# Performance work log

Measured on AMD Instinct MI355X. Metric: run time of the kernel, lower is better.

The kernel has to match this reference:

```python
import jax, jax.numpy as jnp
import numpy as np

V, EH, EO, H, O = 32000, 512, 256, 512, 256
S, B = 128, 32
THRESH = 1e-6


def _uniform(key, shape, fan_in):
    bound = 1.0 / np.sqrt(fan_in)
    return jax.random.uniform(key, shape, jnp.float32, -bound, bound)


def setup_inputs() -> dict:
    key = jax.random.key(0)
    ks = jax.random.split(key, 12)
    return {
        "input": jax.random.randint(ks[0], (S, B), 0, V, dtype=jnp.int32),
        # embedding_layer: Linear(V,EH), Linear(EH,EO); stored (in,out)
        "W1": _uniform(ks[1], (V, EH), V),
        "b1": _uniform(ks[2], (EH,), V),
        "W2": _uniform(ks[3], (EH, EO), EH),
        "b2": _uniform(ks[4], (EO,), EH),
        # GRU weights (PyTorch layout: gates stacked r,z,n)
        "W_ih": _uniform(ks[5], (3 * H, EO), H),
        "W_hh": _uniform(ks[6], (3 * H, H), H),
        "b_ih": _uniform(ks[7], (3 * H,), H),
        "b_hh": _uniform(ks[8], (3 * H,), H),
        # head: Linear(H,O)
        "W3": _uniform(ks[9], (H, O), H),
        "b3": _uniform(ks[10], (O,), H),
    }


def reference(input, W1, b1, W2, b2, W_ih, W_hh, b_ih, b_hh, W3, b3):
    thr = lambda x: jnp.where(x > THRESH, x, 0.0)  # nn.Threshold(1e-6, 0)
    # one_hot(input, V) @ W1 == row gather of W1 (same math, no O(V) GEMM)
    emb = thr(thr(W1[input] + b1) @ W2 + b2)  # (S, B, EO)

    # GRU: precompute input projections for all timesteps
    x_proj = emb @ W_ih.T + b_ih  # (S, B, 3H)
    h0 = jnp.zeros((B, H), jnp.float32)

    def step(h, xp):
        gh = h @ W_hh.T + b_hh
        xr, xz, xn = jnp.split(xp, 3, axis=-1)
        hr, hz, hn = jnp.split(gh, 3, axis=-1)
        r = jax.nn.sigmoid(xr + hr)
        z = jax.nn.sigmoid(xz + hz)
        n = jnp.tanh(xn + r * hn)
        h_new = (1.0 - z) * n + z * h
        return h_new, None

    hT, _ = jax.lax.scan(step, h0, x_proj)  # final hidden (B, H)
    # linear head on h_n (dropout in eval mode = identity); torch h_n is (1,B,H)
    out = hT[None, :, :] @ W3 + b3  # (1, B, O)
    return out
```

## Files before the change

kernel.cpp:

```cpp
#include <hip/hip_runtime.h>
#include <cstddef>

#define THRESH 1e-6f
#define SPIN_LIMIT (1 << 20)

__device__ __forceinline__ float thrf(float x) { return x > THRESH ? x : 0.0f; }
__device__ __forceinline__ float sigm(float x) { return 1.0f / (1.0f + expf(-x)); }
__device__ __forceinline__ void fma4(float4& c, float a, float4 b) {
    c.x += a * b.x; c.y += a * b.y; c.z += a * b.z; c.w += a * b.w;
}
__device__ __forceinline__ void macc4(float4& a, float4 w, float4 h) {
    a.x += w.x * h.x; a.y += w.y * h.y; a.z += w.z * h.z; a.w += w.w * h.w;
}
__device__ __forceinline__ float hsum4(float4 a) { return a.x + a.y + a.z + a.w; }

__global__ __launch_bounds__(256) void k_embed_gemm(const int* __restrict__ tok,
                                                    const float* __restrict__ W1,
                                                    const float* __restrict__ b1,
                                                    const float* __restrict__ W2,
                                                    const float* __restrict__ b2,
                                                    float* __restrict__ emb) {
    constexpr int BM = 64, BN = 64, BK = 32, K = 512, N = 256;
    __shared__ float As[BK][BM + 1];
    __shared__ float Bs[BK][BN];

    const int tid = threadIdx.x;
    const int bm = blockIdx.x * BM;
    const int bn = blockIdx.y * BN;
    const int tn = (tid & 15) * 4;
    const int tm = (tid >> 4) * 4;

    float acc[4][4] = {};

    for (int k0 = 0; k0 < K; k0 += BK) {
        for (int i = tid; i < BM * BK / 4; i += 256) {
            int c4 = (i & (BK / 4 - 1)) * 4;
            int r  = i / (BK / 4);
            int tv = tok[bm + r];
            float4 v  = *(const float4*)(W1 + (size_t)tv * K + k0 + c4);
            float4 bb = *(const float4*)(b1 + k0 + c4);
            As[c4 + 0][r] = thrf(v.x + bb.x);
            As[c4 + 1][r] = thrf(v.y + bb.y);
            As[c4 + 2][r] = thrf(v.z + bb.z);
            As[c4 + 3][r] = thrf(v.w + bb.w);
        }
        for (int i = tid; i < BK * BN / 4; i += 256) {
            int n4 = (i & 15) * 4;
            int kk = i >> 4;
            *(float4*)&Bs[kk][n4] = *(const float4*)(W2 + (size_t)(k0 + kk) * N + bn + n4);
        }
        __syncthreads();

        for (int k = 0; k < BK; ++k) {
            float a0 = As[k][tm + 0], a1 = As[k][tm + 1];
            float a2 = As[k][tm + 2], a3 = As[k][tm + 3];
            float b0 = Bs[k][tn + 0], b1v = Bs[k][tn + 1];
            float b2v = Bs[k][tn + 2], b3v = Bs[k][tn + 3];
            acc[0][0] += a0 * b0;  acc[0][1] += a0 * b1v;
            acc[0][2] += a0 * b2v; acc[0][3] += a0 * b3v;
            acc[1][0] += a1 * b0;  acc[1][1] += a1 * b1v;
            acc[1][2] += a1 * b2v; acc[1][3] += a1 * b3v;
            acc[2][0] += a2 * b0;  acc[2][1] += a2 * b1v;
            acc[2][2] += a2 * b2v; acc[2][3] += a2 * b3v;
            acc[3][0] += a3 * b0;  acc[3][1] += a3 * b1v;
            acc[3][2] += a3 * b2v; acc[3][3] += a3 * b3v;
        }
        __syncthreads();
    }

    const float4 bv = *(const float4*)(b2 + bn + tn);
    for (int i = 0; i < 4; ++i) {
        int m = bm + tm + i;
        float4 o;
        o.x = thrf(acc[i][0] + bv.x);
        o.y = thrf(acc[i][1] + bv.y);
        o.z = thrf(acc[i][2] + bv.z);
        o.w = thrf(acc[i][3] + bv.w);
        *(float4*)(emb + (size_t)m * N + bn + tn) = o;
    }
}

__global__ __launch_bounds__(256) void k_xproj(const float* __restrict__ emb,
                                               const float* __restrict__ W_ih,
                                               const float* __restrict__ b_ih,
                                               float* __restrict__ xp) {
    constexpr int BM = 128, BJ = 64, BK = 32, K = 256, J = 1536;
    __shared__ __align__(16) float As[BK][BM + 4];
    __shared__ __align__(16) float Bs[BK][BJ + 4];
    const int tid = threadIdx.x;
    const int bm = blockIdx.x * BM;
    const int bj = blockIdx.y * BJ;
    const int tj = (tid & 15) * 4;
    const int tm = (tid >> 4) * 8;

    float4 acc[8];
#pragma unroll
    for (int i = 0; i < 8; ++i) acc[i] = make_float4(0.f, 0.f, 0.f, 0.f);

    for (int k0 = 0; k0 < K; k0 += BK) {
#pragma unroll
        for (int p = 0; p < 4; ++p) {
            int i = tid + p * 256;
            int c4 = (i & 7) * 4, r = i >> 3;
            float4 v = *(const float4*)(emb + (size_t)(bm + r) * K + k0 + c4);
            As[c4 + 0][r] = v.x; As[c4 + 1][r] = v.y;
            As[c4 + 2][r] = v.z; As[c4 + 3][r] = v.w;
        }
#pragma unroll
        for (int p = 0; p < 2; ++p) {
            int i = tid + p * 256;
            int c4 = (i & 7) * 4, r = i >> 3;
            float4 v = *(const float4*)(W_ih + (size_t)(bj + r) * K + k0 + c4);
            Bs[c4 + 0][r] = v.x; Bs[c4 + 1][r] = v.y;
            Bs[c4 + 2][r] = v.z; Bs[c4 + 3][r] = v.w;
        }
        __syncthreads();

#pragma unroll 8
        for (int k = 0; k < BK; ++k) {
            float4 b4 = *(const float4*)&Bs[k][tj];
            float4 a0 = *(const float4*)&As[k][tm];
            float4 a1 = *(const float4*)&As[k][tm + 4];
            fma4(acc[0], a0.x, b4); fma4(acc[1], a0.y, b4);
            fma4(acc[2], a0.z, b4); fma4(acc[3], a0.w, b4);
            fma4(acc[4], a1.x, b4); fma4(acc[5], a1.y, b4);
            fma4(acc[6], a1.z, b4); fma4(acc[7], a1.w, b4);
        }
        __syncthreads();
    }

    const float4 bb = *(const float4*)(b_ih + bj + tj);
#pragma unroll
    for (int i = 0; i < 8; ++i) {
        float4 o = make_float4(acc[i].x + bb.x, acc[i].y + bb.y,
                               acc[i].z + bb.z, acc[i].w + bb.w);
        *(float4*)(xp + (size_t)(bm + tm + i) * J + bj + tj) = o;
    }
}

__global__ __launch_bounds__(256) void k_scan(const float* __restrict__ xp,
                                              const float* __restrict__ W_hh,
                                              const float* __restrict__ b_hh,
                                              unsigned long long* __restrict__ hx,
                                              float* __restrict__ h_out) {
    constexpr int HS = 520;
    __shared__ __align__(16) float hl[4][HS];
    __shared__ float red[4][16][12];

    const int tid = threadIdx.x;
    const int g   = blockIdx.x & 7;
    const int m   = blockIdx.x >> 3;
    const int jl  = tid & 15;
    const int kc  = tid >> 4;
    const int jglob = m * 16 + jl;

    float4 wr[8], wz[8], wn[8];
#pragma unroll
    for (int i = 0; i < 8; ++i) {
        const int k = kc * 4 + i * 64;
        wr[i] = *(const float4*)(W_hh + (size_t)jglob * 512 + k);
        wz[i] = *(const float4*)(W_hh + (size_t)(512 + jglob) * 512 + k);
        wn[i] = *(const float4*)(W_hh + (size_t)(1024 + jglob) * 512 + k);
    }

    const int jf  = tid & 15;
    const int bf  = (tid >> 4) & 3;
    const int jfg = m * 16 + jf;
    const int bg  = g * 4 + bf;
    float bhr = 0.f, bhz = 0.f, bhn = 0.f, hprev = 0.f;
    if (tid < 64) {
        bhr = b_hh[jfg];
        bhz = b_hh[512 + jfg];
        bhn = b_hh[1024 + jfg];
    }

    for (int i = tid; i < 4 * HS; i += 256) ((float*)hl)[i] = 0.f;
    __syncthreads();

    for (int t = 0; t < 128; ++t) {
        float xr = 0.f, xz = 0.f, xn = 0.f;
        if (tid < 64) {
            const float* xrow = xp + (size_t)(t * 32 + bg) * 1536;
            xr = xrow[jfg];
            xz = xrow[512 + jfg];
            xn = xrow[1024 + jfg];
        }

        if (t > 0) {
            const unsigned tag = (unsigned)t;
            unsigned long long* base = hx + (size_t)(t & 1) * 16384 + (size_t)(g * 4) * 512;
            unsigned long long v[8];
#pragma unroll
            for (int p = 0; p < 8; ++p)
                v[p] = __hip_atomic_load(base + tid + 256 * p,
                                         __ATOMIC_RELAXED, __HIP_MEMORY_SCOPE_AGENT);
            int spins = 0;
            for (;;) {
                bool all = true;
#pragma unroll
                for (int p = 0; p < 8; ++p) {
                    if ((unsigned)(v[p] >> 32) != tag) {
                        all = false;
                        v[p] = __hip_atomic_load(base + tid + 256 * p,
                                                 __ATOMIC_RELAXED, __HIP_MEMORY_SCOPE_AGENT);
                    }
                }
                if (all || ++spins > SPIN_LIMIT) break;
                __builtin_amdgcn_s_sleep(1);
            }
#pragma unroll
            for (int p = 0; p < 8; ++p) {
                const int flat = tid + 256 * p;
                union { unsigned u; float f; } cv;
                cv.u = (unsigned)v[p];
                hl[flat >> 9][flat & 511] = cv.f;
            }
            __syncthreads();
        }

        float p[3][4];
#pragma unroll
        for (int b = 0; b < 4; ++b) {
            float4 ar = make_float4(0.f, 0.f, 0.f, 0.f), az = ar, an = ar;
#pragma unroll
            for (int i = 0; i < 8; ++i) {
                float4 h4 = *(const float4*)&hl[b][kc * 4 + i * 64];
                macc4(ar, wr[i], h4);
                macc4(az, wz[i], h4);
                macc4(an, wn[i], h4);
            }
            p[0][b] = hsum4(ar); p[1][b] = hsum4(az); p[2][b] = hsum4(an);
        }

#pragma unroll
        for (int gg = 0; gg < 3; ++gg)
#pragma unroll
            for (int b = 0; b < 4; ++b) {
                float v = p[gg][b];
                v += __shfl_xor(v, 16);
                v += __shfl_xor(v, 32);
                p[gg][b] = v;
            }
        if ((tid & 48) == 0) {
            const int w = tid >> 6;
#pragma unroll
            for (int gg = 0; gg < 3; ++gg)
#pragma unroll
                for (int b = 0; b < 4; ++b)
                    red[w][jl][gg * 4 + b] = p[gg][b];
        }
        __syncthreads();

        if (tid < 64) {
            float sr = bhr, sz = bhz, sn = bhn;
#pragma unroll
            for (int w = 0; w < 4; ++w) {
                sr += red[w][jf][0 + bf];
                sz += red[w][jf][4 + bf];
                sn += red[w][jf][8 + bf];
            }
            float r  = sigm(xr + sr);
            float z  = sigm(xz + sz);
            float n  = tanhf(xn + r * sn);
            float hn = (1.0f - z) * n + z * hprev;
            hprev = hn;
            if (t < 127) {
                union { float f; unsigned u; } cv;
                cv.f = hn;
                const unsigned long long pk =
                    ((unsigned long long)(unsigned)(t + 1) << 32) | cv.u;
                __hip_atomic_store(hx + (size_t)((t + 1) & 1) * 16384 + (size_t)bg * 512 + jfg,
                                   pk, __ATOMIC_RELAXED, __HIP_MEMORY_SCOPE_AGENT);
            } else {
                h_out[(size_t)bg * 512 + jfg] = hn;
            }
        }
    }
}

__global__ __launch_bounds__(256) void k_head(const float* __restrict__ h,
                                              const float* __restrict__ W3,
                                              const float* __restrict__ b3,
                                              float* __restrict__ out) {
    const int b = blockIdx.x;
    const int o = threadIdx.x;
    const float* hrow = h + (size_t)b * 512;
    float acc = b3[o];
#pragma unroll 8
    for (int k = 0; k < 512; ++k)
        acc += hrow[k] * W3[(size_t)k * 256 + o];
    out[(size_t)b * 256 + o] = acc;
}

extern "C" void kernel_launch(void* const* d_in, const int* in_sizes, int n_in,
                              void* d_out, int out_size, void* d_ws, size_t ws_size,
                              hipStream_t stream) {
    const int*   tok  = (const int*)d_in[0];
    const float* W1   = (const float*)d_in[1];
    const float* b1   = (const float*)d_in[2];
    const float* W2   = (const float*)d_in[3];
    const float* b2   = (const float*)d_in[4];
    const float* W_ih = (const float*)d_in[5];
    const float* W_hh = (const float*)d_in[6];
    const float* b_ih = (const float*)d_in[7];
    const float* b_hh = (const float*)d_in[8];
    const float* W3   = (const float*)d_in[9];
    const float* b3   = (const float*)d_in[10];
    float* out = (float*)d_out;
    (void)ws_size;

    float* ws   = (float*)d_ws;
    float* emb  = ws;
    float* xp   = ws + 1048576;
    unsigned long long* hx = (unsigned long long*)(ws + 7340032);
    float* hfin = ws + 7340032 + 65536;

    {
        dim3 grd(4096 / 64, 256 / 64);
        k_embed_gemm<<<grd, 256, 0, stream>>>(tok, W1, b1, W2, b2, emb);
    }
    {
        dim3 grd(4096 / 128, 1536 / 64);
        k_xproj<<<grd, 256, 0, stream>>>(emb, W_ih, b_ih, xp);
    }
    k_scan<<<256, 256, 0, stream>>>(xp, W_hh, b_hh, hx, hfin);

    k_head<<<32, 256, 0, stream>>>(hfin, W3, b3, out);
}
```

Measured before the change: 708.7 us.

## Restructure GRU scan: 512-thread blocks, in-wave reduction, double-buffered hidden state

The persistent GRU scan moves from 256 blocks of 256 threads to 128 blocks of 512. Each wave now owns 4 hidden units, and the K dimension is split across 16 lanes, so the gate dot products are reduced with wave shuffles. This removes the shared-memory reduction array and one block barrier per timestep. The hidden state is staged in double-buffered, padded LDS with float4 stores, so only one barrier per step remains. The trade-off is fewer blocks, which means fewer producers and consumers per sync, but more threads per block and more shuffle steps.

Result: slower. 940.3 us (+32.7%).

```diff
diff --git a/kernel.cpp b/kernel.cpp
--- a/kernel.cpp
+++ b/kernel.cpp
@@ -138,93 +138,93 @@
     }
 }
 
-__global__ __launch_bounds__(256) void k_scan(const float* __restrict__ xp,
+__global__ __launch_bounds__(512) void k_scan(const float* __restrict__ xp,
                                               const float* __restrict__ W_hh,
                                               const float* __restrict__ b_hh,
                                               unsigned long long* __restrict__ hx,
                                               float* __restrict__ h_out) {
-    constexpr int HS = 520;
-    __shared__ __align__(16) float hl[4][HS];
-    __shared__ float red[4][16][12];
-
-    const int tid = threadIdx.x;
-    const int g   = blockIdx.x & 7;
-    const int m   = blockIdx.x >> 3;
-    const int jl  = tid & 15;
-    const int kc  = tid >> 4;
-    const int jglob = m * 16 + jl;
+    constexpr int CH = 576;
+    __shared__ __align__(16) float hl[2][4 * CH];
+    const int tid  = threadIdx.x;
+    const int g    = blockIdx.x & 7;
+    const int m    = blockIdx.x >> 3;
+    const int lane = tid & 63;
+    const int wave = tid >> 6;
+    const int kc   = lane & 15;
+    const int jlow = lane >> 4;
+    const int jglob = m * 32 + wave * 4 + jlow;
+    const int hoff  = kc * 36;
 
     float4 wr[8], wz[8], wn[8];
 #pragma unroll
     for (int i = 0; i < 8; ++i) {
-        const int k = kc * 4 + i * 64;
+        const int k = kc * 32 + i * 4;
         wr[i] = *(const float4*)(W_hh + (size_t)jglob * 512 + k);
         wz[i] = *(const float4*)(W_hh + (size_t)(512 + jglob) * 512 + k);
         wn[i] = *(const float4*)(W_hh + (size_t)(1024 + jglob) * 512 + k);
     }
 
-    const int jf  = tid & 15;
-    const int bf  = (tid >> 4) & 3;
-    const int jfg = m * 16 + jf;
-    const int bg  = g * 4 + bf;
+    const int bg = g * 4 + kc;
     float bhr = 0.f, bhz = 0.f, bhn = 0.f, hprev = 0.f;
-    if (tid < 64) {
-        bhr = b_hh[jfg];
-        bhz = b_hh[512 + jfg];
-        bhn = b_hh[1024 + jfg];
-    }
-
-    for (int i = tid; i < 4 * HS; i += 256) ((float*)hl)[i] = 0.f;
-    __syncthreads();
+    if (kc < 4) {
+        bhr = b_hh[jglob];
+        bhz = b_hh[512 + jglob];
+        bhn = b_hh[1024 + jglob];
+    }
+
+    for (int i = tid; i < 4 * CH; i += 512) hl[0][i] = 0.f;
+
+    const int sflat = tid * 4;
+    const int sb = sflat >> 9, sk = sflat & 511;
+    const int sdst = sb * CH + sk + ((sk >> 5) << 2);
 
     for (int t = 0; t < 128; ++t) {
         float xr = 0.f, xz = 0.f, xn = 0.f;
-        if (tid < 64) {
+        if (kc < 4) {
             const float* xrow = xp + (size_t)(t * 32 + bg) * 1536;
-            xr = xrow[jfg];
-            xz = xrow[512 + jfg];
-            xn = xrow[1024 + jfg];
+            xr = xrow[jglob];
+            xz = xrow[512 + jglob];
+            xn = xrow[1024 + jglob];
         }
 
         if (t > 0) {
             const unsigned tag = (unsigned)t;
-            unsigned long long* base = hx + (size_t)(t & 1) * 16384 + (size_t)(g * 4) * 512;
-            unsigned long long v[8];
-#pragma unroll
-            for (int p = 0; p < 8; ++p)
-                v[p] = __hip_atomic_load(base + tid + 256 * p,
-                                         __ATOMIC_RELAXED, __HIP_MEMORY_SCOPE_AGENT);
+            unsigned long long* base = hx + (size_t)(t & 1) * 16384
+                                          + (size_t)(g * 4) * 512 + sflat;
+            unsigned long long v0 = __hip_atomic_load(base + 0, __ATOMIC_RELAXED, __HIP_MEMORY_SCOPE_AGENT);
+            unsigned long long v1 = __hip_atomic_load(base + 1, __ATOMIC_RELAXED, __HIP_MEMORY_SCOPE_AGENT);
+            unsigned long long v2 = __hip_atomic_load(base + 2, __ATOMIC_RELAXED, __HIP_MEMORY_SCOPE_AGENT);
+            unsigned long long v3 = __hip_atomic_load(base + 3, __ATOMIC_RELAXED, __HIP_MEMORY_SCOPE_AGENT);
             int spins = 0;
-            for (;;) {
-                bool all = true;
-#pragma unroll
-                for (int p = 0; p < 8; ++p) {
-                    if ((unsigned)(v[p] >> 32) != tag) {
-                        all = false;
-                        v[p] = __hip_atomic_load(base + tid + 256 * p,
-                                                 __ATOMIC_RELAXED, __HIP_MEMORY_SCOPE_AGENT);
-                    }
-                }
-                if (all || ++spins > SPIN_LIMIT) break;
+            while (((unsigned)(v0 >> 32) != tag) | ((unsigned)(v1 >> 32) != tag) |
+                   ((unsigned)(v2 >> 32) != tag) | ((unsigned)(v3 >> 32) != tag)) {
+                if ((unsigned)(v0 >> 32) != tag)
+                    v0 = __hip_atomic_load(base + 0, __ATOMIC_RELAXED, __HIP_MEMORY_SCOPE_AGENT);
+                if ((unsigned)(v1 >> 32) != tag)
+                    v1 = __hip_atomic_load(base + 1, __ATOMIC_RELAXED, __HIP_MEMORY_SCOPE_AGENT);
+                if ((unsigned)(v2 >> 32) != tag)
+                    v2 = __hip_atomic_load(base + 2, __ATOMIC_RELAXED, __HIP_MEMORY_SCOPE_AGENT);
+                if ((unsigned)(v3 >> 32) != tag)
+                    v3 = __hip_atomic_load(base + 3, __ATOMIC_RELAXED, __HIP_MEMORY_SCOPE_AGENT);
+                if (++spins > SPIN_LIMIT) break;
                 __builtin_amdgcn_s_sleep(1);
             }
-#pragma unroll
-            for (int p = 0; p < 8; ++p) {
-                const int flat = tid + 256 * p;
-                union { unsigned u; float f; } cv;
-                cv.u = (unsigned)v[p];
-                hl[flat >> 9][flat & 511] = cv.f;
-            }
-            __syncthreads();
-        }
-
+            union { unsigned u; float f; } c0, c1, c2, c3;
+            c0.u = (unsigned)v0; c1.u = (unsigned)v1;
+            c2.u = (unsigned)v2; c3.u = (unsigned)v3;
+            *(float4*)&hl[t & 1][sdst] = make_float4(c0.f, c1.f, c2.f, c3.f);
+        }
+        __syncthreads();
+
+        const float* hb = hl[t & 1];
         float p[3][4];
 #pragma unroll
         for (int b = 0; b < 4; ++b) {
             float4 ar = make_float4(0.f, 0.f, 0.f, 0.f), az = ar, an = ar;
+            const float* h0 = hb + b * CH + hoff;
 #pragma unroll
             for (int i = 0; i < 8; ++i) {
-                float4 h4 = *(const float4*)&hl[b][kc * 4 + i * 64];
+                float4 h4 = *(const float4*)(h0 + i * 4);
                 macc4(ar, wr[i], h4);
                 macc4(az, wz[i], h4);
                 macc4(an, wn[i], h4);
@@ -237,42 +237,32 @@
 #pragma unroll
             for (int b = 0; b < 4; ++b) {
                 float v = p[gg][b];
-                v += __shfl_xor(v, 16);
-                v += __shfl_xor(v, 32);
+                v += __shfl_xor(v, 1);
+                v += __shfl_xor(v, 2);
+                v += __shfl_xor(v, 4);
+                v += __shfl_xor(v, 8);
                 p[gg][b] = v;
             }
-        if ((tid & 48) == 0) {
-            const int w = tid >> 6;
-#pragma unroll
-            for (int gg = 0; gg < 3; ++gg)
-#pragma unroll
-                for (int b = 0; b < 4; ++b)
-                    red[w][jl][gg * 4 + b] = p[gg][b];
-        }
-        __syncthreads();
-
-        if (tid < 64) {
-            float sr = bhr, sz = bhz, sn = bhn;
-#pragma unroll
-            for (int w = 0; w < 4; ++w) {
-                sr += red[w][jf][0 + bf];
-                sz += red[w][jf][4 + bf];
-                sn += red[w][jf][8 + bf];
-            }
-            float r  = sigm(xr + sr);
-            float z  = sigm(xz + sz);
-            float n  = tanhf(xn + r * sn);
+
+        if (kc < 4) {
+            float sr, sz, sn;
+            if      (kc == 0) { sr = p[0][0]; sz = p[1][0]; sn = p[2][0]; }
+            else if (kc == 1) { sr = p[0][1]; sz = p[1][1]; sn = p[2][1]; }
+            else if (kc == 2) { sr = p[0][2]; sz = p[1][2]; sn = p[2][2]; }
+            else              { sr = p[0][3]; sz = p[1][3]; sn = p[2][3]; }
+            float r  = sigm(xr + sr + bhr);
+            float z  = sigm(xz + sz + bhz);
+            float n  = tanhf(xn + r * (sn + bhn));
             float hn = (1.0f - z) * n + z * hprev;
             hprev = hn;
             if (t < 127) {
-                union { float f; unsigned u; } cv;
-                cv.f = hn;
-                const unsigned long long pk =
-                    ((unsigned long long)(unsigned)(t + 1) << 32) | cv.u;
-                __hip_atomic_store(hx + (size_t)((t + 1) & 1) * 16384 + (size_t)bg * 512 + jfg,
-                                   pk, __ATOMIC_RELAXED, __HIP_MEMORY_SCOPE_AGENT);
+                union { float f; unsigned u; } cv; cv.f = hn;
+                __hip_atomic_store(hx + (size_t)((t + 1) & 1) * 16384
+                                      + (size_t)bg * 512 + jglob,
+                                   ((unsigned long long)(unsigned)(t + 1) << 32) | cv.u,
+                                   __ATOMIC_RELAXED, __HIP_MEMORY_SCOPE_AGENT);
             } else {
-                h_out[(size_t)bg * 512 + jfg] = hn;
+                h_out[(size_t)bg * 512 + jglob] = hn;
             }
         }
     }
@@ -323,7 +313,7 @@
         dim3 grd(4096 / 128, 1536 / 64);
         k_xproj<<<grd, 256, 0, stream>>>(emb, W_ih, b_ih, xp);
     }
-    k_scan<<<256, 256, 0, stream>>>(xp, W_hh, b_hh, hx, hfin);
+    k_scan<<<128, 512, 0, stream>>>(xp, W_hh, b_hh, hx, hfin);
 
     k_head<<<32, 256, 0, stream>>>(hfin, W3, b3, out);
 }
```

## Fuse GRU input projection into recurrent scan kernel with prefetched embeddings

Applied to the files above, without the earlier changes.

Removes the separate x-projection GEMM kernel and its 25MB intermediate buffer. Each scan block now keeps its 48-row slice of W_ih in shared memory and, while the recurrence runs, computes the next timestep's input projection from a prefetched, double-buffered embedding tile. The aim is to drop a kernel launch and the global traffic for xp, and to hide the projection work behind the cross-block wait. In exchange, 64 threads do a serial 256-long dot product inside the latency-critical recurrence loop. Shared memory use also grows by about 50KB per block.

Result: slower. 920.4 us (+29.9%).

```diff
diff --git a/kernel.cpp b/kernel.cpp
--- a/kernel.cpp
+++ b/kernel.cpp
@@ -6,9 +6,6 @@
 
 __device__ __forceinline__ float thrf(float x) { return x > THRESH ? x : 0.0f; }
 __device__ __forceinline__ float sigm(float x) { return 1.0f / (1.0f + expf(-x)); }
-__device__ __forceinline__ void fma4(float4& c, float a, float4 b) {
-    c.x += a * b.x; c.y += a * b.y; c.z += a * b.z; c.w += a * b.w;
-}
 __device__ __forceinline__ void macc4(float4& a, float4 w, float4 h) {
     a.x += w.x * h.x; a.y += w.y * h.y; a.z += w.z * h.z; a.w += w.w * h.w;
 }
@@ -80,72 +77,19 @@
     }
 }
 
-__global__ __launch_bounds__(256) void k_xproj(const float* __restrict__ emb,
-                                               const float* __restrict__ W_ih,
-                                               const float* __restrict__ b_ih,
-                                               float* __restrict__ xp) {
-    constexpr int BM = 128, BJ = 64, BK = 32, K = 256, J = 1536;
-    __shared__ __align__(16) float As[BK][BM + 4];
-    __shared__ __align__(16) float Bs[BK][BJ + 4];
-    const int tid = threadIdx.x;
-    const int bm = blockIdx.x * BM;
-    const int bj = blockIdx.y * BJ;
-    const int tj = (tid & 15) * 4;
-    const int tm = (tid >> 4) * 8;
-
-    float4 acc[8];
-#pragma unroll
-    for (int i = 0; i < 8; ++i) acc[i] = make_float4(0.f, 0.f, 0.f, 0.f);
-
-    for (int k0 = 0; k0 < K; k0 += BK) {
-#pragma unroll
-        for (int p = 0; p < 4; ++p) {
-            int i = tid + p * 256;
-            int c4 = (i & 7) * 4, r = i >> 3;
-            float4 v = *(const float4*)(emb + (size_t)(bm + r) * K + k0 + c4);
-            As[c4 + 0][r] = v.x; As[c4 + 1][r] = v.y;
-            As[c4 + 2][r] = v.z; As[c4 + 3][r] = v.w;
-        }
-#pragma unroll
-        for (int p = 0; p < 2; ++p) {
-            int i = tid + p * 256;
-            int c4 = (i & 7) * 4, r = i >> 3;
-            float4 v = *(const float4*)(W_ih + (size_t)(bj + r) * K + k0 + c4);
-            Bs[c4 + 0][r] = v.x; Bs[c4 + 1][r] = v.y;
-            Bs[c4 + 2][r] = v.z; Bs[c4 + 3][r] = v.w;
-        }
-        __syncthreads();
-
-#pragma unroll 8
-        for (int k = 0; k < BK; ++k) {
-            float4 b4 = *(const float4*)&Bs[k][tj];
-            float4 a0 = *(const float4*)&As[k][tm];
-            float4 a1 = *(const float4*)&As[k][tm + 4];
-            fma4(acc[0], a0.x, b4); fma4(acc[1], a0.y, b4);
-            fma4(acc[2], a0.z, b4); fma4(acc[3], a0.w, b4);
-            fma4(acc[4], a1.x, b4); fma4(acc[5], a1.y, b4);
-            fma4(acc[6], a1.z, b4); fma4(acc[7], a1.w, b4);
-        }
-        __syncthreads();
-    }
-
-    const float4 bb = *(const float4*)(b_ih + bj + tj);
-#pragma unroll
-    for (int i = 0; i < 8; ++i) {
-        float4 o = make_float4(acc[i].x + bb.x, acc[i].y + bb.y,
-                               acc[i].z + bb.z, acc[i].w + bb.w);
-        *(float4*)(xp + (size_t)(bm + tm + i) * J + bj + tj) = o;
-    }
-}
-
-__global__ __launch_bounds__(256) void k_scan(const float* __restrict__ xp,
+__global__ __launch_bounds__(256) void k_scan(const float* __restrict__ emb,
                                               const float* __restrict__ W_hh,
+                                              const float* __restrict__ W_ih,
                                               const float* __restrict__ b_hh,
+                                              const float* __restrict__ b_ih,
                                               unsigned long long* __restrict__ hx,
                                               float* __restrict__ h_out) {
     constexpr int HS = 520;
     __shared__ __align__(16) float hl[4][HS];
     __shared__ float red[4][16][12];
+    __shared__ __align__(16) float Wx[48][260];
+    __shared__ __align__(16) float el[2][4][260];
+    __shared__ float xl[2][3][64];
 
     const int tid = threadIdx.x;
     const int g   = blockIdx.x & 7;
@@ -163,28 +107,49 @@
         wn[i] = *(const float4*)(W_hh + (size_t)(1024 + jglob) * 512 + k);
     }
 
+    for (int idx = tid; idx < 48 * 64; idx += 256) {
+        const int rr = idx >> 6, c4 = (idx & 63) * 4;
+        const int row = (rr >> 4) * 512 + m * 16 + (rr & 15);
+        *(float4*)&Wx[rr][c4] = *(const float4*)(W_ih + (size_t)row * 256 + c4);
+    }
+    {
+        const int rr = tid >> 6, c4 = (tid & 63) * 4;
+        *(float4*)&el[0][rr][c4] = *(const float4*)(emb + (size_t)(g * 4 + rr) * 256 + c4);
+    }
+
     const int jf  = tid & 15;
     const int bf  = (tid >> 4) & 3;
     const int jfg = m * 16 + jf;
     const int bg  = g * 4 + bf;
     float bhr = 0.f, bhz = 0.f, bhn = 0.f, hprev = 0.f;
+    float bxr = 0.f, bxz = 0.f, bxn = 0.f;
     if (tid < 64) {
-        bhr = b_hh[jfg];
-        bhz = b_hh[512 + jfg];
-        bhn = b_hh[1024 + jfg];
+        bhr = b_hh[jfg];        bhz = b_hh[512 + jfg];  bhn = b_hh[1024 + jfg];
+        bxr = b_ih[jfg];        bxz = b_ih[512 + jfg];  bxn = b_ih[1024 + jfg];
     }
 
     for (int i = tid; i < 4 * HS; i += 256) ((float*)hl)[i] = 0.f;
     __syncthreads();
 
+    if (tid < 64) {
+        float4 a0 = make_float4(0,0,0,0), a1 = a0, a2 = a0;
+#pragma unroll 8
+        for (int i = 0; i < 64; ++i) {
+            const float4 e = *(const float4*)&el[0][bf][i * 4];
+            macc4(a0, *(const float4*)&Wx[jf][i * 4],       e);
+            macc4(a1, *(const float4*)&Wx[16 + jf][i * 4],  e);
+            macc4(a2, *(const float4*)&Wx[32 + jf][i * 4],  e);
+        }
+        xl[0][0][bf * 16 + jf] = hsum4(a0) + bxr;
+        xl[0][1][bf * 16 + jf] = hsum4(a1) + bxz;
+        xl[0][2][bf * 16 + jf] = hsum4(a2) + bxn;
+    }
+
     for (int t = 0; t < 128; ++t) {
-        float xr = 0.f, xz = 0.f, xn = 0.f;
-        if (tid < 64) {
-            const float* xrow = xp + (size_t)(t * 32 + bg) * 1536;
-            xr = xrow[jfg];
-            xz = xrow[512 + jfg];
-            xn = xrow[1024 + jfg];
-        }
+        const int err = tid >> 6, ec4 = (tid & 63) * 4;
+        float4 epf = make_float4(0.f, 0.f, 0.f, 0.f);
+        if (t < 127)
+            epf = *(const float4*)(emb + (size_t)((t + 1) * 32 + g * 4 + err) * 256 + ec4);
 
         if (t > 0) {
             const unsigned tag = (unsigned)t;
@@ -215,8 +180,10 @@
                 cv.u = (unsigned)v[p];
                 hl[flat >> 9][flat & 511] = cv.f;
             }
-            __syncthreads();
-        }
+        }
+        __syncthreads();
+
+        if (t < 127) *(float4*)&el[(t + 1) & 1][err][ec4] = epf;
 
         float p[3][4];
 #pragma unroll
@@ -259,21 +226,38 @@
                 sz += red[w][jf][4 + bf];
                 sn += red[w][jf][8 + bf];
             }
+            const float xr = xl[t & 1][0][bf * 16 + jf];
+            const float xz = xl[t & 1][1][bf * 16 + jf];
+            const float xn = xl[t & 1][2][bf * 16 + jf];
             float r  = sigm(xr + sr);
             float z  = sigm(xz + sz);
             float n  = tanhf(xn + r * sn);
             float hn = (1.0f - z) * n + z * hprev;
             hprev = hn;
             if (t < 127) {
-                union { float f; unsigned u; } cv;
-                cv.f = hn;
-                const unsigned long long pk =
-                    ((unsigned long long)(unsigned)(t + 1) << 32) | cv.u;
-                __hip_atomic_store(hx + (size_t)((t + 1) & 1) * 16384 + (size_t)bg * 512 + jfg,
-                                   pk, __ATOMIC_RELAXED, __HIP_MEMORY_SCOPE_AGENT);
+                union { float f; unsigned u; } cv; cv.f = hn;
+                __hip_atomic_store(hx + (size_t)((t + 1) & 1) * 16384
+                                      + (size_t)bg * 512 + jfg,
+                                   ((unsigned long long)(unsigned)(t + 1) << 32) | cv.u,
+                                   __ATOMIC_RELAXED, __HIP_MEMORY_SCOPE_AGENT);
             } else {
                 h_out[(size_t)bg * 512 + jfg] = hn;
             }
+        }
+
+        if (t < 127 && tid < 64) {
+            const int par = (t + 1) & 1;
+            float4 a0 = make_float4(0,0,0,0), a1 = a0, a2 = a0;
+#pragma unroll 8
+            for (int i = 0; i < 64; ++i) {
+                const float4 e = *(const float4*)&el[par][bf][i * 4];
+                macc4(a0, *(const float4*)&Wx[jf][i * 4],       e);
+                macc4(a1, *(const float4*)&Wx[16 + jf][i * 4],  e);
+                macc4(a2, *(const float4*)&Wx[32 + jf][i * 4],  e);
+            }
+            xl[par][0][bf * 16 + jf] = hsum4(a0) + bxr;
+            xl[par][1][bf * 16 + jf] = hsum4(a1) + bxz;
+            xl[par][2][bf * 16 + jf] = hsum4(a2) + bxn;
         }
     }
 }
@@ -311,19 +295,14 @@
 
     float* ws   = (float*)d_ws;
     float* emb  = ws;
-    float* xp   = ws + 1048576;
-    unsigned long long* hx = (unsigned long long*)(ws + 7340032);
-    float* hfin = ws + 7340032 + 65536;
+    unsigned long long* hx = (unsigned long long*)(ws + 1048576);
+    float* hfin = ws + 1048576 + 131072;
 
     {
         dim3 grd(4096 / 64, 256 / 64);
         k_embed_gemm<<<grd, 256, 0, stream>>>(tok, W1, b1, W2, b2, emb);
     }
-    {
-        dim3 grd(4096 / 128, 1536 / 64);
-        k_xproj<<<grd, 256, 0, stream>>>(emb, W_ih, b_ih, xp);
-    }
-    k_scan<<<256, 256, 0, stream>>>(xp, W_hh, b_hh, hx, hfin);
+    k_scan<<<256, 256, 0, stream>>>(emb, W_hh, W_ih, b_hh, b_ih, hx, hfin);
 
     k_head<<<32, 256, 0, stream>>>(hfin, W3, b3, out);
 }
```
